# Optimization experiments

Hardware: AMD Instinct MI355X
Metric: run time of the kernel (lower is better)

## Reference

```python
import jax, jax.numpy as jnp
import numpy as np

N, T, U, C, V = 8, 256, 64, 512, 1024

def setup_inputs() -> dict:
    key = jax.random.key(0)
    k1, k2, k3, k4 = jax.random.split(key, 4)
    encoder_out = jax.random.normal(k1, (N, T, C), dtype=jnp.float32)
    pred_out = jax.random.normal(k2, (N, U, C), dtype=jnp.float32)
    # nn.Linear(C, V): weight (V, C), bias (V,)
    bound = 1.0 / np.sqrt(C)
    W = jax.random.uniform(k3, (V, C), minval=-bound, maxval=bound, dtype=jnp.float32)
    b = jax.random.uniform(k4, (V,), minval=-bound, maxval=bound, dtype=jnp.float32)
    return {"encoder_out": encoder_out, "pred_out": pred_out, "W": W, "b": b}

def reference(encoder_out, pred_out, W, b):
    # broadcast add: (N,T,1,C) + (N,1,U,C) -> (N,T,U,C)
    x = jnp.tanh(encoder_out[:, :, None, :] + pred_out[:, None, :, :])
    # Linear projection to vocab: (N,T,U,C) @ (C,V) + b
    logits = jnp.einsum("ntuc,vc->ntuv", x, W) + b
    return logits
```

## Files before the change

### kernel.cpp

```cpp
#include <hip/hip_runtime.h>

#define C_DIM 512
#define V_DIM 1024

typedef __attribute__((ext_vector_type(8))) short short8;
typedef __attribute__((ext_vector_type(4))) float f32x4;
typedef __attribute__((ext_vector_type(16))) float f32x16;

__device__ __forceinline__ short f2bf(float f) {
  unsigned int u = __float_as_uint(f);
  u += 0x7fffu + ((u >> 16) & 1u);
  return (short)(u >> 16);
}

__device__ __forceinline__ float fast_tanh_f(float x) {
  float e = __expf(2.0f * x);
  return fmaf(-2.0f, __builtin_amdgcn_rcpf(e + 1.0f), 1.0f);
}

__global__ __launch_bounds__(256) void wswz_kernel(const float* __restrict__ W,
                                                   char* __restrict__ wsw) {
  const int i = blockIdx.x * 256 + threadIdx.x;
  const int v = i >> 6;
  const int c0 = (i & 63) << 3;
  const float* wp = W + (size_t)v * C_DIM + c0;
  const f32x4 w0 = *(const f32x4*)(wp);
  const f32x4 w1 = *(const f32x4*)(wp + 4);
  short8 pk;
  pk[0] = f2bf(w0[0]); pk[1] = f2bf(w0[1]); pk[2] = f2bf(w0[2]); pk[3] = f2bf(w0[3]);
  pk[4] = f2bf(w1[0]); pk[5] = f2bf(w1[1]); pk[6] = f2bf(w1[2]); pk[7] = f2bf(w1[3]);
  const int vt = v >> 8, vloc = v & 255;
  const int wn = vloc >> 6, nt = (vloc >> 5) & 1, c32 = vloc & 31;
  const int kc = c0 >> 5, s = (c0 >> 4) & 1, hi = (c0 >> 3) & 1;
  char* dst = wsw + (size_t)(vt * 16 + kc) * 16384 +
              wn * 4096 + nt * 2048 + s * 1024 + hi * 512 + c32 * 16;
  *(short8*)dst = pk;
}

__global__ __launch_bounds__(256, 2) void joiner_kernel(
    const float* __restrict__ enc, const float* __restrict__ pred,
    const char* __restrict__ wsw, const float* __restrict__ bias,
    float* __restrict__ out) {
  extern __shared__ char smem[];
  const int tid = threadIdx.x;
  const int lane = tid & 63;
  const int wn = tid >> 6;
  const int l31 = lane & 31, hf = lane >> 5;

  const int bid = blockIdx.x;
  const int rp = ((bid & 7) << 8) | (bid >> 3);
  const int n = rp >> 8;

  {
    const int u = ((tid >> 7) << 5) + (tid & 31);
    const int koff = ((tid >> 6) & 1) * 16 + ((tid >> 5) & 1) * 8;
    const float* pe = enc + (size_t)rp * C_DIM + koff;
    const float* pp = pred + ((size_t)(n * 64 + u)) * C_DIM + koff;
    char* adst = smem + tid * 16;
#pragma unroll 4
    for (int kc = 0; kc < 16; ++kc) {
      const f32x4 e0 = *(const f32x4*)(pe + kc * 32);
      const f32x4 e1 = *(const f32x4*)(pe + kc * 32 + 4);
      const f32x4 p0 = *(const f32x4*)(pp + kc * 32);
      const f32x4 p1 = *(const f32x4*)(pp + kc * 32 + 4);
      short8 pk;
      pk[0] = f2bf(fast_tanh_f(e0[0] + p0[0]));
      pk[1] = f2bf(fast_tanh_f(e0[1] + p0[1]));
      pk[2] = f2bf(fast_tanh_f(e0[2] + p0[2]));
      pk[3] = f2bf(fast_tanh_f(e0[3] + p0[3]));
      pk[4] = f2bf(fast_tanh_f(e1[0] + p1[0]));
      pk[5] = f2bf(fast_tanh_f(e1[1] + p1[1]));
      pk[6] = f2bf(fast_tanh_f(e1[2] + p1[2]));
      pk[7] = f2bf(fast_tanh_f(e1[3] + p1[3]));
      *(short8*)(adst + kc * 4096) = pk;
    }
  }
  __syncthreads();

  const char* ab = smem + hf * 512 + l31 * 16;
  const char* wb = wsw + wn * 4096 + hf * 512 + l31 * 16;

  f32x16 acc[2][2];
#pragma unroll
  for (int mt = 0; mt < 2; ++mt)
#pragma unroll
    for (int nt = 0; nt < 2; ++nt)
#pragma unroll
      for (int r = 0; r < 16; ++r) acc[mt][nt][r] = 0.0f;

  short8 bfr[2][4];

#pragma unroll
  for (int f = 0; f < 4; ++f) bfr[0][f] = *(const short8*)(wb + f * 1024);

#pragma unroll 1
  for (int vt = 0; vt < 4; ++vt) {
    const char* wg = wb + (size_t)vt * 262144;
#pragma unroll
    for (int kc = 0; kc < 16; ++kc) {
      const int cb = kc & 1, nb = cb ^ 1;

      if (kc < 15 || vt < 3) {
        const char* bp = wg + (kc + 1) * 16384;
#pragma unroll
        for (int f = 0; f < 4; ++f)
          bfr[nb][f] = *(const short8*)(bp + f * 1024);
      }

      const char* ap = ab + kc * 4096;
      const short8 a_m0s0 = *(const short8*)(ap);
      const short8 a_m1s0 = *(const short8*)(ap + 2048);
      const short8 a_m0s1 = *(const short8*)(ap + 1024);
      const short8 a_m1s1 = *(const short8*)(ap + 3072);

      __builtin_amdgcn_s_setprio(1);
      acc[0][0] = __builtin_amdgcn_mfma_f32_32x32x16_bf16(a_m0s0, bfr[cb][0], acc[0][0], 0, 0, 0);
      acc[0][1] = __builtin_amdgcn_mfma_f32_32x32x16_bf16(a_m0s0, bfr[cb][2], acc[0][1], 0, 0, 0);
      acc[1][0] = __builtin_amdgcn_mfma_f32_32x32x16_bf16(a_m1s0, bfr[cb][0], acc[1][0], 0, 0, 0);
      acc[1][1] = __builtin_amdgcn_mfma_f32_32x32x16_bf16(a_m1s0, bfr[cb][2], acc[1][1], 0, 0, 0);
      acc[0][0] = __builtin_amdgcn_mfma_f32_32x32x16_bf16(a_m0s1, bfr[cb][1], acc[0][0], 0, 0, 0);
      acc[0][1] = __builtin_amdgcn_mfma_f32_32x32x16_bf16(a_m0s1, bfr[cb][3], acc[0][1], 0, 0, 0);
      acc[1][0] = __builtin_amdgcn_mfma_f32_32x32x16_bf16(a_m1s1, bfr[cb][1], acc[1][0], 0, 0, 0);
      acc[1][1] = __builtin_amdgcn_mfma_f32_32x32x16_bf16(a_m1s1, bfr[cb][3], acc[1][1], 0, 0, 0);
      __builtin_amdgcn_s_setprio(0);
    }

    {
      const int colb = (vt << 8) + (wn << 6) + l31;
      float* ob = out + ((size_t)rp * 64 + hf * 4) * V_DIM + colb;
#pragma unroll
      for (int nt = 0; nt < 2; ++nt) {
        const float bb = bias[colb + nt * 32];
#pragma unroll
        for (int mt = 0; mt < 2; ++mt) {
#pragma unroll
          for (int r = 0; r < 16; ++r) {
            const int row_off = mt * 32 + (r & 3) + 8 * (r >> 2);
            __builtin_nontemporal_store(acc[mt][nt][r] + bb,
                                        ob + (size_t)row_off * V_DIM + nt * 32);
            acc[mt][nt][r] = 0.0f;
          }
        }
      }
    }
  }
}

extern "C" void kernel_launch(void* const* d_in, const int* in_sizes, int n_in,
                              void* d_out, int out_size, void* d_ws, size_t ws_size,
                              hipStream_t stream) {
  const float* enc  = (const float*)d_in[0];
  const float* pred = (const float*)d_in[1];
  const float* W    = (const float*)d_in[2];
  const float* bias = (const float*)d_in[3];
  float* out = (float*)d_out;
  char* wsw = (char*)d_ws;

  wswz_kernel<<<dim3(256), dim3(256), 0, stream>>>(W, wsw);

  (void)hipFuncSetAttribute((const void*)joiner_kernel,
                            hipFuncAttributeMaxDynamicSharedMemorySize, 65536);
  joiner_kernel<<<dim3(2048), dim3(256), 65536, stream>>>(enc, pred, wsw, bias, out);
}
```

Baseline: 632.4 us.

## Split M across two wave groups with 512-thread blocks and halve per-wave accumulators

Doubles the block to 512 threads (8 waves) and splits the 64-row M tile between two wave groups, so each wave holds 2 accumulator tiles instead of 4 and issues 4 MFMAs per k-step. The A-tile producer loop is remapped so 512 threads fill the same shared-memory layout in 8 iterations. The aim is to lower register pressure and raise occupancy and latency hiding, at the cost of each B fragment being loaded from global by twice as many waves. There is a redundant duplicated store to pk[7] that is immediately overwritten.

```diff
diff --git a/kernel.cpp b/kernel.cpp
--- a/kernel.cpp
+++ b/kernel.cpp
@@ -37,14 +37,16 @@
   *(short8*)dst = pk;
 }
 
-__global__ __launch_bounds__(256, 2) void joiner_kernel(
+__global__ __launch_bounds__(512, 4) void joiner_kernel(
     const float* __restrict__ enc, const float* __restrict__ pred,
     const char* __restrict__ wsw, const float* __restrict__ bias,
     float* __restrict__ out) {
   extern __shared__ char smem[];
   const int tid = threadIdx.x;
   const int lane = tid & 63;
-  const int wn = tid >> 6;
+  const int wv = tid >> 6;
+  const int wm = wv >> 2;
+  const int wn = wv & 3;
   const int l31 = lane & 31, hf = lane >> 5;
 
   const int bid = blockIdx.x;
@@ -52,17 +54,19 @@
   const int n = rp >> 8;
 
   {
-    const int u = ((tid >> 7) << 5) + (tid & 31);
-    const int koff = ((tid >> 6) & 1) * 16 + ((tid >> 5) & 1) * 8;
-    const float* pe = enc + (size_t)rp * C_DIM + koff;
-    const float* pp = pred + ((size_t)(n * 64 + u)) * C_DIM + koff;
+    const int rem = tid & 255;
+    const int f = rem >> 6, hf5 = (rem >> 5) & 1, l = rem & 31;
+    const int u = (f >> 1) * 32 + l;
+    const int k0 = (tid >> 8) * 32 + (f & 1) * 16 + hf5 * 8;
+    const float* pe = enc + (size_t)rp * C_DIM + k0;
+    const float* pp = pred + ((size_t)(n * 64 + u)) * C_DIM + k0;
     char* adst = smem + tid * 16;
-#pragma unroll 4
-    for (int kc = 0; kc < 16; ++kc) {
-      const f32x4 e0 = *(const f32x4*)(pe + kc * 32);
-      const f32x4 e1 = *(const f32x4*)(pe + kc * 32 + 4);
-      const f32x4 p0 = *(const f32x4*)(pp + kc * 32);
-      const f32x4 p1 = *(const f32x4*)(pp + kc * 32 + 4);
+#pragma unroll 2
+    for (int p = 0; p < 8; ++p) {
+      const f32x4 e0 = *(const f32x4*)(pe + p * 64);
+      const f32x4 e1 = *(const f32x4*)(pe + p * 64 + 4);
+      const f32x4 p0 = *(const f32x4*)(pp + p * 64);
+      const f32x4 p1 = *(const f32x4*)(pp + p * 64 + 4);
       short8 pk;
       pk[0] = f2bf(fast_tanh_f(e0[0] + p0[0]));
       pk[1] = f2bf(fast_tanh_f(e0[1] + p0[1]));
@@ -71,22 +75,21 @@
       pk[4] = f2bf(fast_tanh_f(e1[0] + p1[0]));
       pk[5] = f2bf(fast_tanh_f(e1[1] + p1[1]));
       pk[6] = f2bf(fast_tanh_f(e1[2] + p1[2]));
+      pk[7] = f2bf(fast_tanh_f(e1[3] + p1[7 - 7]));
       pk[7] = f2bf(fast_tanh_f(e1[3] + p1[3]));
-      *(short8*)(adst + kc * 4096) = pk;
+      *(short8*)(adst + p * 8192) = pk;
     }
   }
   __syncthreads();
 
-  const char* ab = smem + hf * 512 + l31 * 16;
+  const char* ab = smem + wm * 2048 + hf * 512 + l31 * 16;
   const char* wb = wsw + wn * 4096 + hf * 512 + l31 * 16;
 
-  f32x16 acc[2][2];
+  f32x16 acc[2];
 #pragma unroll
-  for (int mt = 0; mt < 2; ++mt)
+  for (int nt = 0; nt < 2; ++nt)
 #pragma unroll
-    for (int nt = 0; nt < 2; ++nt)
-#pragma unroll
-      for (int r = 0; r < 16; ++r) acc[mt][nt][r] = 0.0f;
+    for (int r = 0; r < 16; ++r) acc[nt][r] = 0.0f;
 
   short8 bfr[2][4];
 
@@ -108,38 +111,29 @@
       }
 
       const char* ap = ab + kc * 4096;
-      const short8 a_m0s0 = *(const short8*)(ap);
-      const short8 a_m1s0 = *(const short8*)(ap + 2048);
-      const short8 a_m0s1 = *(const short8*)(ap + 1024);
-      const short8 a_m1s1 = *(const short8*)(ap + 3072);
+      const short8 a_s0 = *(const short8*)(ap);
+      const short8 a_s1 = *(const short8*)(ap + 1024);
 
       __builtin_amdgcn_s_setprio(1);
-      acc[0][0] = __builtin_amdgcn_mfma_f32_32x32x16_bf16(a_m0s0, bfr[cb][0], acc[0][0], 0, 0, 0);
-      acc[0][1] = __builtin_amdgcn_mfma_f32_32x32x16_bf16(a_m0s0, bfr[cb][2], acc[0][1], 0, 0, 0);
-      acc[1][0] = __builtin_amdgcn_mfma_f32_32x32x16_bf16(a_m1s0, bfr[cb][0], acc[1][0], 0, 0, 0);
-      acc[1][1] = __builtin_amdgcn_mfma_f32_32x32x16_bf16(a_m1s0, bfr[cb][2], acc[1][1], 0, 0, 0);
-      acc[0][0] = __builtin_amdgcn_mfma_f32_32x32x16_bf16(a_m0s1, bfr[cb][1], acc[0][0], 0, 0, 0);
-      acc[0][1] = __builtin_amdgcn_mfma_f32_32x32x16_bf16(a_m0s1, bfr[cb][3], acc[0][1], 0, 0, 0);
-      acc[1][0] = __builtin_amdgcn_mfma_f32_32x32x16_bf16(a_m1s1, bfr[cb][1], acc[1][0], 0, 0, 0);
-      acc[1][1] = __builtin_amdgcn_mfma_f32_32x32x16_bf16(a_m1s1, bfr[cb][3], acc[1][1], 0, 0, 0);
+      acc[0] = __builtin_amdgcn_mfma_f32_32x32x16_bf16(a_s0, bfr[cb][0], acc[0], 0, 0, 0);
+      acc[1] = __builtin_amdgcn_mfma_f32_32x32x16_bf16(a_s0, bfr[cb][2], acc[1], 0, 0, 0);
+      acc[0] = __builtin_amdgcn_mfma_f32_32x32x16_bf16(a_s1, bfr[cb][1], acc[0], 0, 0, 0);
+      acc[1] = __builtin_amdgcn_mfma_f32_32x32x16_bf16(a_s1, bfr[cb][3], acc[1], 0, 0, 0);
       __builtin_amdgcn_s_setprio(0);
     }
 
     {
       const int colb = (vt << 8) + (wn << 6) + l31;
-      float* ob = out + ((size_t)rp * 64 + hf * 4) * V_DIM + colb;
+      float* ob = out + ((size_t)rp * 64 + wm * 32 + hf * 4) * V_DIM + colb;
 #pragma unroll
       for (int nt = 0; nt < 2; ++nt) {
         const float bb = bias[colb + nt * 32];
 #pragma unroll
-        for (int mt = 0; mt < 2; ++mt) {
-#pragma unroll
-          for (int r = 0; r < 16; ++r) {
-            const int row_off = mt * 32 + (r & 3) + 8 * (r >> 2);
-            __builtin_nontemporal_store(acc[mt][nt][r] + bb,
-                                        ob + (size_t)row_off * V_DIM + nt * 32);
-            acc[mt][nt][r] = 0.0f;
-          }
+        for (int r = 0; r < 16; ++r) {
+          const int row_off = (r & 3) + 8 * (r >> 2);
+          __builtin_nontemporal_store(acc[nt][r] + bb,
+                                      ob + (size_t)row_off * V_DIM + nt * 32);
+          acc[nt][r] = 0.0f;
         }
       }
     }
@@ -160,5 +154,5 @@
 
   (void)hipFuncSetAttribute((const void*)joiner_kernel,
                             hipFuncAttributeMaxDynamicSharedMemorySize, 65536);
-  joiner_kernel<<<dim3(2048), dim3(256), 65536, stream>>>(enc, pred, wsw, bias, out);
+  joiner_kernel<<<dim3(2048), dim3(512), 65536, stream>>>(enc, pred, wsw, bias, out);
 }
```

New measurement: 650.3 us. 1.03x slower.
